# Kernel tuning notes

Measured on AMD Instinct MI355X. Metric: run time of the kernel, lower is better.

The kernel has to match this reference:

```python
import jax, jax.numpy as jnp
import numpy as np

K = 3          # kernel size
STRIDE = 2
PAD = 1
DIL = 1
SHAPE = 128    # input spatial extent per axis
B = 2          # batch size
N = 100000     # active input voxels
CIN = 32
COUT = 64
OUT = (SHAPE + 2 * PAD - DIL * (K - 1) - 1) // STRIDE + 1  # 64


def setup_inputs() -> dict:
    key = jax.random.key(0)
    kf, kw, kc, kb = jax.random.split(key, 4)
    features = jax.random.normal(kf, (N, CIN), jnp.float32)
    W = jax.random.normal(kw, (K, K, K, CIN, COUT), jnp.float32) * 0.05
    xyz = jax.random.randint(kc, (N, 3), 0, SHAPE, jnp.int32)
    b = jax.random.randint(kb, (N, 1), 0, B, jnp.int32)
    coors = jnp.concatenate([b, xyz], axis=1)  # [N, 4] = (batch, z, y, x)
    return {"features": features, "W": W, "coors": coors, "batch_size": B}


def reference(features, W, coors, batch_size):
    # Sparse 3D conv via gather-GEMM-scatter per kernel offset.
    # Output voxel o receives input p iff p = o*stride - pad + k*dil, i.e.
    # o = (p + pad - k*dil) / stride when divisible and in range.
    bidx = coors[:, 0].astype(jnp.int32)          # [N]
    pos = coors[:, 1:4].astype(jnp.int32)         # [N, 3]
    out = jnp.zeros((batch_size * OUT * OUT * OUT, COUT), features.dtype)
    for kz in range(K):
        for ky in range(K):
            for kx in range(K):
                off = jnp.array([kz, ky, kx], jnp.int32)
                num = pos + PAD - off * DIL        # [N, 3]
                o = num // STRIDE                  # candidate output coords
                valid = jnp.all((num % STRIDE == 0) & (o >= 0) & (o < OUT), axis=1)
                flat = ((bidx * OUT + o[:, 0]) * OUT + o[:, 1]) * OUT + o[:, 2]
                flat = jnp.where(valid, flat, 0)
                contrib = jnp.where(valid[:, None], features, 0.0) @ W[kz, ky, kx]
                out = out.at[flat].add(contrib)
    # Densified sparse-conv output: active sites hold exact spconv values,
    # inactive sites are zero (no contributions).
    return out.reshape(batch_size, OUT, OUT, OUT, COUT)
```

## Files before the change

### kernel.cpp

```cpp
#include <hip/hip_runtime.h>


#define CIN   32
#define COUT  64
#define OUTD  64
#define NBLK  2048
#define NPTS  128

__device__ __forceinline__ int axis_opts(int p, int* k, int* o) {
    int cnt = 0;
    const int kp = (p + 1) & 1;
    const int o0 = (p + 1 - kp) >> 1;
    if (o0 < OUTD) { k[cnt] = kp; o[cnt] = o0; ++cnt; }
    if (kp == 0) {
        const int o1 = o0 - 1;
        if (o1 >= 0) { k[cnt] = 2; o[cnt] = o1; ++cnt; }
    }
    return cnt;
}

__global__ void conv_w_bf16(const float* __restrict__ W, ushort* __restrict__ wsW)
{
    const int k = blockIdx.x;
    for (int i = threadIdx.x; i < CIN * COUT; i += 256) {
        const int c = i >> 6, ch = i & 63;
        const unsigned u = __float_as_uint(W[k * CIN * COUT + i]);
        const unsigned r = (u + 0x7fffu + ((u >> 16) & 1u)) >> 16;
        wsW[(k << 11) + (ch << 5) + c] = (ushort)r;
    }
}

__global__ __launch_bounds__(256) void scatter2(
    const float* __restrict__ feats, const ushort* __restrict__ wsW,
    const int4* __restrict__ coors, float* __restrict__ out,
    int N, int totWaves)
{
    const int ch = threadIdx.x & 63;
    const int wv = __builtin_amdgcn_readfirstlane(threadIdx.x >> 6);
    const int gwave = blockIdx.x * 4 + wv;

    for (int i = gwave; i < N; i += totWaves) {
        const int4 c = coors[i];
        const float4* fp = (const float4*)(feats + (size_t)i * CIN);
        float4 f[8];
        #pragma unroll
        for (int q = 0; q < 8; ++q) f[q] = fp[q];

        int kz[2], oz[2], ky[2], oy[2], kx[2], ox[2];
        const int nz = axis_opts(c.y, kz, oz);
        const int ny = axis_opts(c.z, ky, oy);
        const int nx = axis_opts(c.w, kx, ox);

        for (int az = 0; az < nz; ++az)
        for (int ay = 0; ay < ny; ++ay)
        for (int ax = 0; ax < nx; ++ax) {
            const int kidx = (kz[az] * 3 + ky[ay]) * 3 + kx[ax];
            const uint4* wp = (const uint4*)(wsW + (kidx << 11) + (ch << 5));
            uint4 w4[4];
            #pragma unroll
            for (int q = 0; q < 4; ++q) w4[q] = wp[q];
            float s0 = 0.f, s1 = 0.f;
            #pragma unroll
            for (int q = 0; q < 4; ++q) {
                const uint4 wq = w4[q];
                const float4 fa = f[2 * q], fb = f[2 * q + 1];
                s0 += fa.x * __uint_as_float(wq.x << 16);
                s1 += fa.y * __uint_as_float(wq.x & 0xffff0000u);
                s0 += fa.z * __uint_as_float(wq.y << 16);
                s1 += fa.w * __uint_as_float(wq.y & 0xffff0000u);
                s0 += fb.x * __uint_as_float(wq.z << 16);
                s1 += fb.y * __uint_as_float(wq.z & 0xffff0000u);
                s0 += fb.z * __uint_as_float(wq.w << 16);
                s1 += fb.w * __uint_as_float(wq.w & 0xffff0000u);
            }
            const size_t flat = (((size_t)c.x * OUTD + oz[az]) * OUTD + oy[ay]) * OUTD + ox[ax];
            unsafeAtomicAdd(out + flat * COUT + ch, s0 + s1);
        }
    }
}

__global__ __launch_bounds__(256, 4) void spconv_scatter(
    const float* __restrict__ feats, const float* __restrict__ Wt,
    const int* __restrict__ coors, float* __restrict__ out, int N)
{
    __shared__ float sf[NPTS][CIN];
    __shared__ int   sc[NPTS][4];
    __shared__ int   vf[NPTS];

    const int tid = threadIdx.x;
    const int ch  = tid & 63;
    const int wv  = tid >> 6;
    const int base = blockIdx.x * NPTS;
    const int npts = min(NPTS, (int)(N - base));
    if (npts <= 0) return;

    for (int i = tid; i < npts * CIN; i += 256) sf[0][i] = feats[base * CIN + i];
    for (int i = tid; i < npts * 4; i += 256) ((int*)sc)[i] = coors[base * 4 + i];
    __syncthreads();

    for (int off = 0; off < 27; ++off) {
        const int kz = off / 9, ky = (off / 3) % 3, kx = off % 3;
        if (tid < npts) {
            const int p  = tid;
            const int nz = sc[p][1] + 1 - kz;
            const int ny = sc[p][2] + 1 - ky;
            const int nx = sc[p][3] + 1 - kx;
            const int m  = nz | ny | nx;
            const int oz = nz >> 1, oy = ny >> 1, ox = nx >> 1;
            const bool v = ((m & 0x80000001) == 0) &&
                           (oz < OUTD) && (oy < OUTD) && (ox < OUTD);
            vf[p] = v ? (((sc[p][0] * OUTD + oz) * OUTD + oy) * OUTD + ox) : -1;
        }
        const float* wp = Wt + off * (CIN * COUT) + ch;
        float w[CIN];
        #pragma unroll
        for (int c = 0; c < CIN; ++c) w[c] = wp[c * COUT];
        __syncthreads();
        for (int p = wv; p < npts; p += 4) {
            const int f = vf[p];
            if (f >= 0) {
                float s = 0.f;
                #pragma unroll
                for (int c = 0; c < CIN; ++c) s += sf[p][c] * w[c];
                atomicAdd(&out[(size_t)f * COUT + ch], s);
            }
        }
        __syncthreads();
    }
}

extern "C" void kernel_launch(void* const* d_in, const int* in_sizes, int n_in,
                              void* d_out, int out_size, void* d_ws, size_t ws_size,
                              hipStream_t stream) {
    const float* feats = (const float*)d_in[0];
    const float* Wt    = (const float*)d_in[1];
    const int*   coors = (const int*)d_in[2];
    float*       out   = (float*)d_out;

    const int N = in_sizes[0] / CIN;

    hipMemsetAsync(d_out, 0, (size_t)out_size * sizeof(float), stream);

    const size_t need = 27 * CIN * COUT * sizeof(ushort);
    if (ws_size >= need) {
        ushort* wsW = (ushort*)d_ws;
        conv_w_bf16<<<27, 256, 0, stream>>>(Wt, wsW);
        const int NB = NBLK;
        scatter2<<<NB, 256, 0, stream>>>(feats, wsW, (const int4*)coors, out, N, NB * 4);
    } else {
        spconv_scatter<<<(N + NPTS - 1) / NPTS, 256, 0, stream>>>(feats, Wt, coors, out, N);
    }
}
```

Baseline: 133.5 us.

## Replace scatter atomics with dense-map gather conv over output tiles

Builds a dense voxel-to-index hash map (with linked lists for duplicate coordinates) in workspace, then runs a gather kernel in which each block owns two 4x4x4 output tiles. Contributions accumulate in shared memory and are written to the output with coalesced float4 stores, so the separate output memset and the global atomics are no longer needed. In exchange it adds a memset of a 16.8M-int map, a build kernel, and random map lookups for every output voxel and kernel offset, most of which hit empty sites. It also relies on the workspace being large enough for the map.

```diff
diff --git a/kernel.cpp b/kernel.cpp
--- a/kernel.cpp
+++ b/kernel.cpp
@@ -4,30 +4,129 @@
 #define CIN   32
 #define COUT  64
 #define OUTD  64
+#define IND   128
+#define TILE  4
+#define GRID  2048
+#define NTH   256
+#define NPTS  128
 #define NBLK  2048
-#define NPTS  128
+
+__global__ void build_map(const int4* __restrict__ coors, int* __restrict__ map,
+                          int* __restrict__ nxt, int N)
+{
+    int i = blockIdx.x * 256 + threadIdx.x;
+    if (i >= N) return;
+    const int4 c = coors[i];
+    const int v = ((c.x * IND + c.y) * IND + c.z) * IND + c.w;
+    nxt[i] = atomicExch(&map[v], i);
+}
+
+__global__ void conv_w_bf16(const float* __restrict__ W, ushort* __restrict__ wsW)
+{
+    const int k = blockIdx.x;
+    for (int i = threadIdx.x; i < CIN * COUT; i += 256) {
+        const int c = i >> 6, chh = i & 63;
+        const unsigned u = __float_as_uint(W[k * CIN * COUT + i]);
+        const unsigned r = (u + 0x7fffu + ((u >> 16) & 1u)) >> 16;
+        wsW[(k << 11) + (chh << 5) + c] = (ushort)r;
+    }
+}
+
+__global__ __launch_bounds__(NTH) void gather_k(
+    const float* __restrict__ feats, const ushort* __restrict__ wsW,
+    const int* __restrict__ map, const int* __restrict__ nxt,
+    float* __restrict__ out, int nUnits)
+{
+    __shared__ float acc[2 * 64 * COUT];
+
+    const int tid = threadIdx.x;
+    const int ch  = tid & 63;
+    const int wv  = tid >> 6;
+    const int vz = ch >> 4, vy = (ch >> 2) & 3, vx = ch & 3;
+
+    for (int u = blockIdx.x; u < nUnits; u += GRID) {
+        for (int i = tid; i < 2 * 64 * COUT; i += NTH) acc[i] = 0.f;
+        __syncthreads();
+
+        for (int k = wv; k < 27; k += 4) {
+            const int kz = k / 9, ky = (k / 3) % 3, kx = k % 3;
+            const uint4* wp = (const uint4*)(wsW + (k << 11) + (ch << 5));
+            uint4 w4[4];
+            #pragma unroll
+            for (int q = 0; q < 4; ++q) w4[q] = wp[q];
+
+            #pragma unroll
+            for (int half = 0; half < 2; ++half) {
+                int tt = 2 * u + half;
+                const int ox0 = (tt & 15) * TILE; tt >>= 4;
+                const int oy0 = (tt & 15) * TILE; tt >>= 4;
+                const int oz0 = (tt & 15) * TILE; tt >>= 4;
+                const int b   = tt;
+
+                const int px = 2 * (ox0 + vx) - 1 + kx;
+                const int py = 2 * (oy0 + vy) - 1 + ky;
+                const int pz = 2 * (oz0 + vz) - 1 + kz;
+                int j = -1;
+                if ((unsigned)px < IND && (unsigned)py < IND && (unsigned)pz < IND)
+                    j = map[((b * IND + pz) * IND + py) * IND + px];
+
+                for (unsigned long long m = __ballot(j >= 0); m; m &= m - 1) {
+                    const int L = __builtin_ctzll(m);
+                    int jj = __shfl(j, L);
+                    const int aoff = half * 4096 + L * 64 + ch;
+                    while (jj >= 0) {
+                        const float4* fp = (const float4*)(feats + (size_t)jj * CIN);
+                        float4 f[8];
+                        #pragma unroll
+                        for (int q = 0; q < 8; ++q) f[q] = fp[q];
+                        float s0 = 0.f, s1 = 0.f;
+                        #pragma unroll
+                        for (int q = 0; q < 4; ++q) {
+                            const uint4 wq = w4[q];
+                            const float4 fa = f[2 * q], fb = f[2 * q + 1];
+                            s0 += fa.x * __uint_as_float(wq.x << 16);
+                            s1 += fa.y * __uint_as_float(wq.x & 0xffff0000u);
+                            s0 += fa.z * __uint_as_float(wq.y << 16);
+                            s1 += fa.w * __uint_as_float(wq.y & 0xffff0000u);
+                            s0 += fb.x * __uint_as_float(wq.z << 16);
+                            s1 += fb.y * __uint_as_float(wq.z & 0xffff0000u);
+                            s0 += fb.z * __uint_as_float(wq.w << 16);
+                            s1 += fb.w * __uint_as_float(wq.w & 0xffff0000u);
+                        }
+                        unsafeAtomicAdd(&acc[aoff], s0 + s1);
+                        jj = nxt[jj];
+                    }
+                }
+            }
+        }
+        __syncthreads();
+
+        #pragma unroll
+        for (int it = 0; it < 8; ++it) {
+            const int i4 = (it * NTH + tid) * 4;
+            int tt = 2 * u + (i4 >> 12);
+            const int ox0 = (tt & 15) * TILE; tt >>= 4;
+            const int oy0 = (tt & 15) * TILE; tt >>= 4;
+            const int oz0 = (tt & 15) * TILE; tt >>= 4;
+            const int b   = tt;
+            const int inner = i4 & 4095;
+            const int row = inner >> 8;
+            const int rvz = row >> 2, rvy = row & 3;
+            const int inrow = inner & 255;
+            const size_t g = ((((size_t)b * OUTD + (oz0 + rvz)) * OUTD + (oy0 + rvy)) * OUTD + ox0) * COUT + inrow;
+            *(float4*)(out + g) = *(const float4*)(acc + i4);
+        }
+        __syncthreads();
+    }
+}
 
 __device__ __forceinline__ int axis_opts(int p, int* k, int* o) {
     int cnt = 0;
     const int kp = (p + 1) & 1;
     const int o0 = (p + 1 - kp) >> 1;
     if (o0 < OUTD) { k[cnt] = kp; o[cnt] = o0; ++cnt; }
-    if (kp == 0) {
-        const int o1 = o0 - 1;
-        if (o1 >= 0) { k[cnt] = 2; o[cnt] = o1; ++cnt; }
-    }
+    if (kp == 0) { const int o1 = o0 - 1; if (o1 >= 0) { k[cnt] = 2; o[cnt] = o1; ++cnt; } }
     return cnt;
-}
-
-__global__ void conv_w_bf16(const float* __restrict__ W, ushort* __restrict__ wsW)
-{
-    const int k = blockIdx.x;
-    for (int i = threadIdx.x; i < CIN * COUT; i += 256) {
-        const int c = i >> 6, ch = i & 63;
-        const unsigned u = __float_as_uint(W[k * CIN * COUT + i]);
-        const unsigned r = (u + 0x7fffu + ((u >> 16) & 1u)) >> 16;
-        wsW[(k << 11) + (ch << 5) + c] = (ushort)r;
-    }
 }
 
 __global__ __launch_bounds__(256) void scatter2(
@@ -35,27 +134,24 @@
     const int4* __restrict__ coors, float* __restrict__ out,
     int N, int totWaves)
 {
-    const int ch = threadIdx.x & 63;
+    const int chh = threadIdx.x & 63;
     const int wv = __builtin_amdgcn_readfirstlane(threadIdx.x >> 6);
     const int gwave = blockIdx.x * 4 + wv;
-
     for (int i = gwave; i < N; i += totWaves) {
         const int4 c = coors[i];
         const float4* fp = (const float4*)(feats + (size_t)i * CIN);
         float4 f[8];
         #pragma unroll
         for (int q = 0; q < 8; ++q) f[q] = fp[q];
-
         int kz[2], oz[2], ky[2], oy[2], kx[2], ox[2];
         const int nz = axis_opts(c.y, kz, oz);
         const int ny = axis_opts(c.z, ky, oy);
         const int nx = axis_opts(c.w, kx, ox);
-
         for (int az = 0; az < nz; ++az)
         for (int ay = 0; ay < ny; ++ay)
         for (int ax = 0; ax < nx; ++ax) {
             const int kidx = (kz[az] * 3 + ky[ay]) * 3 + kx[ax];
-            const uint4* wp = (const uint4*)(wsW + (kidx << 11) + (ch << 5));
+            const uint4* wp = (const uint4*)(wsW + (kidx << 11) + (chh << 5));
             uint4 w4[4];
             #pragma unroll
             for (int q = 0; q < 4; ++q) w4[q] = wp[q];
@@ -74,7 +170,7 @@
                 s1 += fb.w * __uint_as_float(wq.w & 0xffff0000u);
             }
             const size_t flat = (((size_t)c.x * OUTD + oz[az]) * OUTD + oy[ay]) * OUTD + ox[ax];
-            unsafeAtomicAdd(out + flat * COUT + ch, s0 + s1);
+            unsafeAtomicAdd(out + flat * COUT + chh, s0 + s1);
         }
     }
 }
@@ -86,18 +182,15 @@
     __shared__ float sf[NPTS][CIN];
     __shared__ int   sc[NPTS][4];
     __shared__ int   vf[NPTS];
-
     const int tid = threadIdx.x;
-    const int ch  = tid & 63;
+    const int chh = tid & 63;
     const int wv  = tid >> 6;
     const int base = blockIdx.x * NPTS;
     const int npts = min(NPTS, (int)(N - base));
     if (npts <= 0) return;
-
     for (int i = tid; i < npts * CIN; i += 256) sf[0][i] = feats[base * CIN + i];
     for (int i = tid; i < npts * 4; i += 256) ((int*)sc)[i] = coors[base * 4 + i];
     __syncthreads();
-
     for (int off = 0; off < 27; ++off) {
         const int kz = off / 9, ky = (off / 3) % 3, kx = off % 3;
         if (tid < npts) {
@@ -111,7 +204,7 @@
                            (oz < OUTD) && (oy < OUTD) && (ox < OUTD);
             vf[p] = v ? (((sc[p][0] * OUTD + oz) * OUTD + oy) * OUTD + ox) : -1;
         }
-        const float* wp = Wt + off * (CIN * COUT) + ch;
+        const float* wp = Wt + off * (CIN * COUT) + chh;
         float w[CIN];
         #pragma unroll
         for (int c = 0; c < CIN; ++c) w[c] = wp[c * COUT];
@@ -122,7 +215,7 @@
                 float s = 0.f;
                 #pragma unroll
                 for (int c = 0; c < CIN; ++c) s += sf[p][c] * w[c];
-                atomicAdd(&out[(size_t)f * COUT + ch], s);
+                atomicAdd(&out[(size_t)f * COUT + chh], s);
             }
         }
         __syncthreads();
@@ -138,16 +231,30 @@
     float*       out   = (float*)d_out;
 
     const int N = in_sizes[0] / CIN;
-
-    hipMemsetAsync(d_out, 0, (size_t)out_size * sizeof(float), stream);
-
-    const size_t need = 27 * CIN * COUT * sizeof(ushort);
-    if (ws_size >= need) {
+    const int B = out_size / (OUTD * OUTD * OUTD * COUT);
+
+    const size_t mapElems = (size_t)B * IND * IND * IND;
+    const size_t nxtPad   = ((size_t)N + 3) & ~(size_t)3;
+    const size_t wOfs     = mapElems + nxtPad;
+    const size_t needMap  = (wOfs + (27 * CIN * COUT + 1) / 2) * sizeof(int);
+    const size_t needBf   = 27 * CIN * COUT * sizeof(ushort);
+
+    if (ws_size >= needMap) {
+        int*    map = (int*)d_ws;
+        int*    nxt = map + mapElems;
+        ushort* wsW = (ushort*)(map + wOfs);
+        hipMemsetAsync(map, 0xFF, mapElems * sizeof(int), stream);
+        build_map<<<(N + 255) / 256, 256, 0, stream>>>((const int4*)coors, map, nxt, N);
+        conv_w_bf16<<<27, 256, 0, stream>>>(Wt, wsW);
+        const int nUnits = (B * 16 * 16 * 16) / 2;
+        gather_k<<<GRID, NTH, 0, stream>>>(feats, wsW, map, nxt, out, nUnits);
+    } else if (ws_size >= needBf) {
+        hipMemsetAsync(d_out, 0, (size_t)out_size * sizeof(float), stream);
         ushort* wsW = (ushort*)d_ws;
         conv_w_bf16<<<27, 256, 0, stream>>>(Wt, wsW);
-        const int NB = NBLK;
-        scatter2<<<NB, 256, 0, stream>>>(feats, wsW, (const int4*)coors, out, N, NB * 4);
+        scatter2<<<NBLK, 256, 0, stream>>>(feats, wsW, (const int4*)coors, out, N, NBLK * 4);
     } else {
+        hipMemsetAsync(d_out, 0, (size_t)out_size * sizeof(float), stream);
         spconv_scatter<<<(N + NPTS - 1) / NPTS, 256, 0, stream>>>(feats, Wt, coors, out, N);
     }
 }
```

After: 195.9 us. +46.8%, slower.
